# Performance work log

Hardware: AMD Instinct MI355X
Metric: run time of the kernel (lower is better)

## Reference

```python
import jax, jax.numpy as jnp
import numpy as np

B = 512          # batch_size
C = 4            # num_classes
N = 16384        # grid unknowns per sample (128x128)
H = 0.0078125    # grid spacing h = 1/128


def setup_inputs() -> dict:
    key = jax.random.key(0)
    k1, k2, k3 = jax.random.split(key, 3)
    coefficients = jax.random.uniform(k1, (B, N), dtype=jnp.float32)  # positive -> A SPD
    predictions = jax.random.normal(k2, (B, C, N), dtype=jnp.float32)
    targets = jax.random.normal(k3, (B, N, C), dtype=jnp.float32)
    return {"coefficients": coefficients, "predictions": predictions, "targets": targets}


def reference(coefficients, predictions, targets):
    # A = diag(h^2 * coefficients[i]); exploit diagonality: A @ v == a * v.
    a = (H * H) * coefficients                      # [B, N] diagonal of A per sample
    preds = predictions.reshape(B, C, -1)           # predictions.view(batch_size, num_classes, -1)

    # Modified Gram-Schmidt in the A-inner product, vectorized over batch.
    ortho = []
    for j in range(C):                              # tiny fixed loop over classes
        v = preds[:, j, :]                          # [B, N]
        for e in ortho:
            proj = jnp.sum(v * (a * e), axis=-1, keepdims=True)  # <v, A e>
            v = v - proj * e
        n2 = jnp.sum(v * a * v, axis=-1, keepdims=True)          # <v, A v>
        safe = jnp.where(n2 > 0, n2, jnp.float32(1.0))
        v = jnp.where(n2 > 0, v * jax.lax.rsqrt(safe), v)        # normalize iff <v,Av> > 0
        ortho.append(v)
    Cm = jnp.stack(ortho, axis=1)                   # [B, C, N]

    # M = C_i @ A @ targets[i] for each sample -> [B, C, C]
    M = jnp.einsum('bcn,bnm->bcm', Cm * a[:, None, :], targets)
    per_sample = (jnp.float32(4.0) - jnp.sum(M * M, axis=(1, 2))) / jnp.float32(4.0)
    return jnp.mean(per_sample)
```

## Files before the change

### kernel.cpp

```cpp
#include <hip/hip_runtime.h>

#define BSZ 512
#define NC  4
#define NN  16384
#define H2  (0.0078125f * 0.0078125f)

#define BLK 512

__device__ __forceinline__ void accum_elem(float a,
                                           float p0, float p1, float p2, float p3,
                                           float tx, float ty, float tz, float tw,
                                           float* acc)
{
    float ap0 = a * p0, ap1 = a * p1, ap2 = a * p2, ap3 = a * p3;
    acc[0]  += ap0 * p0;  acc[1]  += ap0 * p1;  acc[2]  += ap0 * p2;  acc[3]  += ap0 * p3;
    acc[4]  += ap1 * p1;  acc[5]  += ap1 * p2;  acc[6]  += ap1 * p3;
    acc[7]  += ap2 * p2;  acc[8]  += ap2 * p3;
    acc[9]  += ap3 * p3;
    acc[10] += ap0 * tx;  acc[11] += ap0 * ty;  acc[12] += ap0 * tz;  acc[13] += ap0 * tw;
    acc[14] += ap1 * tx;  acc[15] += ap1 * ty;  acc[16] += ap1 * tz;  acc[17] += ap1 * tw;
    acc[18] += ap2 * tx;  acc[19] += ap2 * ty;  acc[20] += ap2 * tz;  acc[21] += ap2 * tw;
    acc[22] += ap3 * tx;  acc[23] += ap3 * ty;  acc[24] += ap3 * tz;  acc[25] += ap3 * tw;
}

__global__ __launch_bounds__(BLK)
void loss_main(const float* __restrict__ coef,
               const float* __restrict__ pred,
               const float* __restrict__ targ,
               float* __restrict__ per_sample)
{
    const int b   = blockIdx.x;
    const int tid = threadIdx.x;

    const float4* __restrict__ c4 = (const float4*)(coef + (size_t)b * NN);
    const float4* __restrict__ q0 = (const float4*)(pred + (size_t)b * NC * NN + 0 * NN);
    const float4* __restrict__ q1 = (const float4*)(pred + (size_t)b * NC * NN + 1 * NN);
    const float4* __restrict__ q2 = (const float4*)(pred + (size_t)b * NC * NN + 2 * NN);
    const float4* __restrict__ q3 = (const float4*)(pred + (size_t)b * NC * NN + 3 * NN);
    const float4* __restrict__ t4 = (const float4*)(targ + (size_t)b * NN * NC);

    float acc[26];
#pragma unroll
    for (int k = 0; k < 26; ++k) acc[k] = 0.f;

    for (int i = tid; i < NN / 4; i += BLK) {
        float4 cc = c4[i];
        float4 a0 = q0[i];
        float4 a1 = q1[i];
        float4 a2 = q2[i];
        float4 a3 = q3[i];
        float4 t0 = t4[4 * i + 0];
        float4 t1 = t4[4 * i + 1];
        float4 t2 = t4[4 * i + 2];
        float4 t3 = t4[4 * i + 3];

        accum_elem(H2 * cc.x, a0.x, a1.x, a2.x, a3.x, t0.x, t0.y, t0.z, t0.w, acc);
        accum_elem(H2 * cc.y, a0.y, a1.y, a2.y, a3.y, t1.x, t1.y, t1.z, t1.w, acc);
        accum_elem(H2 * cc.z, a0.z, a1.z, a2.z, a3.z, t2.x, t2.y, t2.z, t2.w, acc);
        accum_elem(H2 * cc.w, a0.w, a1.w, a2.w, a3.w, t3.x, t3.y, t3.z, t3.w, acc);
    }

    const int lane = tid & 63;
    const int wv   = tid >> 6;
    __shared__ float red[26][8];

#pragma unroll
    for (int k = 0; k < 26; ++k) {
        float v = acc[k];
#pragma unroll
        for (int o = 32; o > 0; o >>= 1) v += __shfl_down(v, o, 64);
        if (lane == 0) red[k][wv] = v;
    }
    __syncthreads();

    if (tid == 0) {
        float s[26];
#pragma unroll
        for (int k = 0; k < 26; ++k) {
            float v = 0.f;
#pragma unroll
            for (int w = 0; w < 8; ++w) v += red[k][w];
            s[k] = v;
        }

        float Gm[4][4];
        Gm[0][0] = s[0];
        Gm[0][1] = Gm[1][0] = s[1];
        Gm[0][2] = Gm[2][0] = s[2];
        Gm[0][3] = Gm[3][0] = s[3];
        Gm[1][1] = s[4];
        Gm[1][2] = Gm[2][1] = s[5];
        Gm[1][3] = Gm[3][1] = s[6];
        Gm[2][2] = s[7];
        Gm[2][3] = Gm[3][2] = s[8];
        Gm[3][3] = s[9];

        float Tm[4][4];
#pragma unroll
        for (int i = 0; i < 4; ++i)
#pragma unroll
            for (int m = 0; m < 4; ++m) Tm[i][m] = s[10 + 4 * i + m];

        float u[4][4];
#pragma unroll
        for (int j = 0; j < 4; ++j) {
            float w[4];
#pragma unroll
            for (int i = 0; i < 4; ++i) w[i] = (i == j) ? 1.f : 0.f;
#pragma unroll
            for (int k = 0; k < 4; ++k) {
                if (k < j) {
                    float proj = 0.f;
#pragma unroll
                    for (int i = 0; i < 4; ++i) {
                        float gu = 0.f;
#pragma unroll
                        for (int l = 0; l < 4; ++l) gu += Gm[i][l] * u[k][l];
                        proj += w[i] * gu;
                    }
#pragma unroll
                    for (int i = 0; i < 4; ++i) w[i] -= proj * u[k][i];
                }
            }
            float n2 = 0.f;
#pragma unroll
            for (int i = 0; i < 4; ++i) {
                float gw = 0.f;
#pragma unroll
                for (int l = 0; l < 4; ++l) gw += Gm[i][l] * w[l];
                n2 += w[i] * gw;
            }
            float sc = (n2 > 0.f) ? rsqrtf(n2) : 1.f;
#pragma unroll
            for (int i = 0; i < 4; ++i) u[j][i] = w[i] * sc;
        }

        float ssum = 0.f;
#pragma unroll
        for (int c = 0; c < 4; ++c) {
#pragma unroll
            for (int m = 0; m < 4; ++m) {
                float M = 0.f;
#pragma unroll
                for (int i = 0; i < 4; ++i) M += u[c][i] * Tm[i][m];
                ssum += M * M;
            }
        }
        per_sample[b] = (4.f - ssum) * 0.25f;
    }
}

__global__ __launch_bounds__(BSZ)
void reduce_final(const float* __restrict__ ps, float* __restrict__ out)
{
    const int tid = threadIdx.x;
    float v = ps[tid];
#pragma unroll
    for (int o = 32; o > 0; o >>= 1) v += __shfl_down(v, o, 64);
    __shared__ float red[8];
    if ((tid & 63) == 0) red[tid >> 6] = v;
    __syncthreads();
    if (tid == 0) {
        float ssum = 0.f;
#pragma unroll
        for (int w = 0; w < 8; ++w) ssum += red[w];
        out[0] = ssum / (float)BSZ;
    }
}

extern "C" void kernel_launch(void* const* d_in, const int* in_sizes, int n_in,
                              void* d_out, int out_size, void* d_ws, size_t ws_size,
                              hipStream_t stream)
{
    const float* coef = (const float*)d_in[0];
    const float* pred = (const float*)d_in[1];
    const float* targ = (const float*)d_in[2];
    float* out = (float*)d_out;
    float* ps  = (float*)d_ws;

    loss_main<<<BSZ, BLK, 0, stream>>>(coef, pred, targ, ps);
    reduce_final<<<1, BSZ, 0, stream>>>(ps, out);
}
```

Before: 303.3 us.

## Split each sample across 4 blocks and move Gram-Schmidt into finalize kernel

Each sample's reduction is now split into 4 segments handled by separate 256-thread blocks, giving 2048 blocks instead of 512, with fully unrolled fixed-trip loads. The partial 26-term sums go to the workspace. A single finalize kernel then sums the segments and runs the 4x4 Gram-Schmidt and loss per sample, one thread per sample. The aim is better occupancy and more memory-level parallelism on a bandwidth-bound stream. The cost is extra workspace traffic and a serial tail in one block.

After: 347.7 us. 14.6% more time.

```diff
diff --git a/kernel.cpp b/kernel.cpp
--- a/kernel.cpp
+++ b/kernel.cpp
@@ -5,7 +5,11 @@
 #define NN  16384
 #define H2  (0.0078125f * 0.0078125f)
 
-#define BLK 512
+#define BLK   256
+#define SSEG  4
+#define NG    (NN / 4)
+#define GSEG  (NG / SSEG)
+#define ITERS (GSEG / BLK)
 
 __device__ __forceinline__ void accum_elem(float a,
                                            float p0, float p1, float p2, float p3,
@@ -23,13 +27,14 @@
     acc[22] += ap3 * tx;  acc[23] += ap3 * ty;  acc[24] += ap3 * tz;  acc[25] += ap3 * tw;
 }
 
-__global__ __launch_bounds__(BLK)
-void loss_main(const float* __restrict__ coef,
-               const float* __restrict__ pred,
-               const float* __restrict__ targ,
-               float* __restrict__ per_sample)
+__global__ __launch_bounds__(BLK, 4)
+void loss_partial(const float* __restrict__ coef,
+                  const float* __restrict__ pred,
+                  const float* __restrict__ targ,
+                  float* __restrict__ ws)
 {
-    const int b   = blockIdx.x;
+    const int seg = blockIdx.x;
+    const int b   = blockIdx.y;
     const int tid = threadIdx.x;
 
     const float4* __restrict__ c4 = (const float4*)(coef + (size_t)b * NN);
@@ -43,16 +48,18 @@
 #pragma unroll
     for (int k = 0; k < 26; ++k) acc[k] = 0.f;
 
-    for (int i = tid; i < NN / 4; i += BLK) {
-        float4 cc = c4[i];
-        float4 a0 = q0[i];
-        float4 a1 = q1[i];
-        float4 a2 = q2[i];
-        float4 a3 = q3[i];
-        float4 t0 = t4[4 * i + 0];
-        float4 t1 = t4[4 * i + 1];
-        float4 t2 = t4[4 * i + 2];
-        float4 t3 = t4[4 * i + 3];
+#pragma unroll
+    for (int it = 0; it < ITERS; ++it) {
+        const int g = seg * GSEG + it * BLK + tid;
+        float4 cc = c4[g];
+        float4 a0 = q0[g];
+        float4 a1 = q1[g];
+        float4 a2 = q2[g];
+        float4 a3 = q3[g];
+        float4 t0 = t4[4 * g + 0];
+        float4 t1 = t4[4 * g + 1];
+        float4 t2 = t4[4 * g + 2];
+        float4 t3 = t4[4 * g + 3];
 
         accum_elem(H2 * cc.x, a0.x, a1.x, a2.x, a3.x, t0.x, t0.y, t0.z, t0.w, acc);
         accum_elem(H2 * cc.y, a0.y, a1.y, a2.y, a3.y, t1.x, t1.y, t1.z, t1.w, acc);
@@ -62,7 +69,7 @@
 
     const int lane = tid & 63;
     const int wv   = tid >> 6;
-    __shared__ float red[26][8];
+    __shared__ float red[26][4];
 
 #pragma unroll
     for (int k = 0; k < 26; ++k) {
@@ -73,98 +80,101 @@
     }
     __syncthreads();
 
-    if (tid == 0) {
-        float s[26];
-#pragma unroll
-        for (int k = 0; k < 26; ++k) {
-            float v = 0.f;
-#pragma unroll
-            for (int w = 0; w < 8; ++w) v += red[k][w];
-            s[k] = v;
-        }
-
-        float Gm[4][4];
-        Gm[0][0] = s[0];
-        Gm[0][1] = Gm[1][0] = s[1];
-        Gm[0][2] = Gm[2][0] = s[2];
-        Gm[0][3] = Gm[3][0] = s[3];
-        Gm[1][1] = s[4];
-        Gm[1][2] = Gm[2][1] = s[5];
-        Gm[1][3] = Gm[3][1] = s[6];
-        Gm[2][2] = s[7];
-        Gm[2][3] = Gm[3][2] = s[8];
-        Gm[3][3] = s[9];
-
-        float Tm[4][4];
-#pragma unroll
-        for (int i = 0; i < 4; ++i)
-#pragma unroll
-            for (int m = 0; m < 4; ++m) Tm[i][m] = s[10 + 4 * i + m];
-
-        float u[4][4];
-#pragma unroll
-        for (int j = 0; j < 4; ++j) {
-            float w[4];
-#pragma unroll
-            for (int i = 0; i < 4; ++i) w[i] = (i == j) ? 1.f : 0.f;
-#pragma unroll
-            for (int k = 0; k < 4; ++k) {
-                if (k < j) {
-                    float proj = 0.f;
-#pragma unroll
-                    for (int i = 0; i < 4; ++i) {
-                        float gu = 0.f;
-#pragma unroll
-                        for (int l = 0; l < 4; ++l) gu += Gm[i][l] * u[k][l];
-                        proj += w[i] * gu;
-                    }
-#pragma unroll
-                    for (int i = 0; i < 4; ++i) w[i] -= proj * u[k][i];
-                }
-            }
-            float n2 = 0.f;
-#pragma unroll
-            for (int i = 0; i < 4; ++i) {
-                float gw = 0.f;
-#pragma unroll
-                for (int l = 0; l < 4; ++l) gw += Gm[i][l] * w[l];
-                n2 += w[i] * gw;
-            }
-            float sc = (n2 > 0.f) ? rsqrtf(n2) : 1.f;
-#pragma unroll
-            for (int i = 0; i < 4; ++i) u[j][i] = w[i] * sc;
-        }
-
-        float ssum = 0.f;
-#pragma unroll
-        for (int c = 0; c < 4; ++c) {
-#pragma unroll
-            for (int m = 0; m < 4; ++m) {
-                float M = 0.f;
-#pragma unroll
-                for (int i = 0; i < 4; ++i) M += u[c][i] * Tm[i][m];
-                ssum += M * M;
-            }
-        }
-        per_sample[b] = (4.f - ssum) * 0.25f;
+    if (tid < 26) {
+        float v = red[tid][0] + red[tid][1] + red[tid][2] + red[tid][3];
+        ws[((size_t)seg * 26 + tid) * BSZ + b] = v;
     }
 }
 
 __global__ __launch_bounds__(BSZ)
-void reduce_final(const float* __restrict__ ps, float* __restrict__ out)
+void finalize(const float* __restrict__ ws, float* __restrict__ out)
 {
-    const int tid = threadIdx.x;
-    float v = ps[tid];
+    const int b = threadIdx.x;
+
+    float s[26];
 #pragma unroll
-    for (int o = 32; o > 0; o >>= 1) v += __shfl_down(v, o, 64);
+    for (int k = 0; k < 26; ++k) s[k] = 0.f;
+#pragma unroll
+    for (int seg = 0; seg < SSEG; ++seg)
+#pragma unroll
+        for (int k = 0; k < 26; ++k)
+            s[k] += ws[((size_t)seg * 26 + k) * BSZ + b];
+
+    float Gm[4][4];
+    Gm[0][0] = s[0];
+    Gm[0][1] = Gm[1][0] = s[1];
+    Gm[0][2] = Gm[2][0] = s[2];
+    Gm[0][3] = Gm[3][0] = s[3];
+    Gm[1][1] = s[4];
+    Gm[1][2] = Gm[2][1] = s[5];
+    Gm[1][3] = Gm[3][1] = s[6];
+    Gm[2][2] = s[7];
+    Gm[2][3] = Gm[3][2] = s[8];
+    Gm[3][3] = s[9];
+
+    float Tm[4][4];
+#pragma unroll
+    for (int i = 0; i < 4; ++i)
+#pragma unroll
+        for (int m = 0; m < 4; ++m) Tm[i][m] = s[10 + 4 * i + m];
+
+    float u[4][4];
+#pragma unroll
+    for (int j = 0; j < 4; ++j) {
+        float w[4];
+#pragma unroll
+        for (int i = 0; i < 4; ++i) w[i] = (i == j) ? 1.f : 0.f;
+#pragma unroll
+        for (int k = 0; k < 4; ++k) {
+            if (k < j) {
+                float proj = 0.f;
+#pragma unroll
+                for (int i = 0; i < 4; ++i) {
+                    float gu = 0.f;
+#pragma unroll
+                    for (int l = 0; l < 4; ++l) gu += Gm[i][l] * u[k][l];
+                    proj += w[i] * gu;
+                }
+#pragma unroll
+                for (int i = 0; i < 4; ++i) w[i] -= proj * u[k][i];
+            }
+        }
+        float n2 = 0.f;
+#pragma unroll
+        for (int i = 0; i < 4; ++i) {
+            float gw = 0.f;
+#pragma unroll
+            for (int l = 0; l < 4; ++l) gw += Gm[i][l] * w[l];
+            n2 += w[i] * gw;
+        }
+        float sc = (n2 > 0.f) ? rsqrtf(n2) : 1.f;
+#pragma unroll
+        for (int i = 0; i < 4; ++i) u[j][i] = w[i] * sc;
+    }
+
+    float ssum = 0.f;
+#pragma unroll
+    for (int c = 0; c < 4; ++c) {
+#pragma unroll
+        for (int m = 0; m < 4; ++m) {
+            float M = 0.f;
+#pragma unroll
+            for (int i = 0; i < 4; ++i) M += u[c][i] * Tm[i][m];
+            ssum += M * M;
+        }
+    }
+    float ps = (4.f - ssum) * 0.25f;
+
+#pragma unroll
+    for (int o = 32; o > 0; o >>= 1) ps += __shfl_down(ps, o, 64);
     __shared__ float red[8];
-    if ((tid & 63) == 0) red[tid >> 6] = v;
+    if ((b & 63) == 0) red[b >> 6] = ps;
     __syncthreads();
-    if (tid == 0) {
-        float ssum = 0.f;
+    if (b == 0) {
+        float t = 0.f;
 #pragma unroll
-        for (int w = 0; w < 8; ++w) ssum += red[w];
-        out[0] = ssum / (float)BSZ;
+        for (int w = 0; w < 8; ++w) t += red[w];
+        out[0] = t / (float)BSZ;
     }
 }
 
@@ -176,8 +186,9 @@
     const float* pred = (const float*)d_in[1];
     const float* targ = (const float*)d_in[2];
     float* out = (float*)d_out;
-    float* ps  = (float*)d_ws;
+    float* ws  = (float*)d_ws;
 
-    loss_main<<<BSZ, BLK, 0, stream>>>(coef, pred, targ, ps);
-    reduce_final<<<1, BSZ, 0, stream>>>(ps, out);
+    dim3 grid(SSEG, BSZ);
+    loss_partial<<<grid, BLK, 0, stream>>>(coef, pred, targ, ws);
+    finalize<<<1, BSZ, 0, stream>>>(ws, out);
 }
```
